# Kernel tuning notes

Hardware: AMD Instinct MI355X
Metric: run time of the kernel (lower is better)

The kernel has to match this reference:

```python
import jax, jax.numpy as jnp
import numpy as np
from jax import lax

EPS = 1e-8  # numerical safety in squash sqrt (torch repo uses plain sqrt)

def squash(s, axis=-1):
    sq = jnp.sum(s * s, axis=axis, keepdims=True)
    return (sq / (1.0 + sq)) * s / jnp.sqrt(sq + EPS)

def conv2d(x, w, b, stride):
    y = lax.conv_general_dilated(x, w, (stride, stride), 'VALID',
                                 dimension_numbers=('NCHW', 'OIHW', 'NCHW'))
    return y + b[None, :, None, None]

def setup_inputs() -> dict:
    key = jax.random.key(0)
    ks = jax.random.split(key, 12)
    B = 256
    x = jax.random.normal(ks[0], (B, 1, 28, 28), dtype=jnp.float32)
    conv_w = jax.random.normal(ks[1], (256, 1, 9, 9), dtype=jnp.float32) * 0.05
    conv_b = jnp.zeros((256,), dtype=jnp.float32)
    caps1_w = jax.random.normal(ks[2], (32, 8, 256, 9, 9), dtype=jnp.float32) * 0.01
    caps1_b = jnp.zeros((32, 8), dtype=jnp.float32)
    caps2_w = jax.random.normal(ks[3], (10, 1152, 8, 16), dtype=jnp.float32)  # torch.randn
    dec_w1 = jax.random.normal(ks[4], (160, 512), dtype=jnp.float32) * 0.05
    dec_b1 = jnp.zeros((512,), dtype=jnp.float32)
    dec_w2 = jax.random.normal(ks[5], (512, 1024), dtype=jnp.float32) * 0.04
    dec_b2 = jnp.zeros((1024,), dtype=jnp.float32)
    dec_w3 = jax.random.normal(ks[6], (1024, 784), dtype=jnp.float32) * 0.03
    dec_b3 = jnp.zeros((784,), dtype=jnp.float32)
    return {"x": x, "conv_w": conv_w, "conv_b": conv_b, "caps1_w": caps1_w,
            "caps1_b": caps1_b, "caps2_w": caps2_w, "dec_w1": dec_w1,
            "dec_b1": dec_b1, "dec_w2": dec_w2, "dec_b2": dec_b2,
            "dec_w3": dec_w3, "dec_b3": dec_b3}

def reference(x, conv_w, conv_b, caps1_w, caps1_b, caps2_w,
              dec_w1, dec_b1, dec_w2, dec_b2, dec_w3, dec_b3):
    B = x.shape[0]
    # conv + relu -> [B,256,20,20]
    h = jax.nn.relu(conv2d(x, conv_w, conv_b, 1))
    # CapsLayerOne: 32 parallel convs folded into one grouped-out conv -> [B,256,6,6]
    u = conv2d(h, caps1_w.reshape(32 * 8, 256, 9, 9), caps1_b.reshape(-1), 2)
    u = u.reshape(B, 32, 8, 6, 6)                    # [B,caps,ch,h,w]
    # replicate torch cat(dim=-1).view(B,8,-1): flatten order (h, caps, w) per channel
    u = u.transpose(0, 2, 3, 1, 4).reshape(B, 8, 1152)  # [B,8,N]
    u = squash(u.transpose(0, 2, 1))                 # [B,N,8], N=1152
    # CapsLayerTwo dynamic routing
    x_hat = jnp.einsum('bni,cnio->cbno', u, caps2_w)[:, :, :, None, :]  # [10,B,N,1,16]
    b = jnp.zeros_like(x_hat)
    v = None
    for i in range(3):
        c = jax.nn.softmax(b, axis=2)
        s = jnp.sum(x_hat * c, axis=2, keepdims=True)  # [10,B,1,1,16]
        v = squash(s)
        if i != 2:
            b = b + jnp.sum(x_hat * v, axis=-1, keepdims=True)
    v = v[:, :, 0, 0, :].transpose(1, 0, 2)            # [B,10,16]
    class_scores = jnp.sqrt(jnp.sum(v * v, axis=-1) + EPS)  # [B,10]
    class_probabilities = jax.nn.softmax(class_scores, axis=-1)
    labels = jnp.argmax(class_probabilities, axis=1)
    y = jax.nn.one_hot(labels, 10, dtype=v.dtype)
    masked = (v * y[:, :, None]).reshape(B, 160)
    d = jax.nn.relu(masked @ dec_w1 + dec_b1)
    d = jax.nn.relu(d @ dec_w2 + dec_b2)
    reconstructions = jax.nn.sigmoid(d @ dec_w3 + dec_b3)  # [B,784]
    return (class_probabilities, reconstructions)
```

## Files before the change

### kernel.cpp

```cpp
#include <hip/hip_runtime.h>
#include <cstdint>
#include <cstddef>

#define EPSF 1e-8f

typedef __attribute__((ext_vector_type(8))) short bf16x8;
typedef __attribute__((ext_vector_type(4))) float f32x4;
typedef unsigned short ushort_t;

static __device__ __forceinline__ ushort_t f2bf(float f) {
  unsigned u = __builtin_bit_cast(unsigned, f);
  unsigned r = (u + 0x7FFFu + ((u >> 16) & 1u)) >> 16;
  return (ushort_t)r;
}
static __device__ __forceinline__ float bf2f(ushort_t h) {
  return __builtin_bit_cast(float, (unsigned)h << 16);
}

__global__ __launch_bounds__(256) void conv1_kernel(
    const float* __restrict__ x, const float* __restrict__ cw,
    const float* __restrict__ cb, ushort_t* __restrict__ h2hi, ushort_t* __restrict__ h2lo)
{
  int oy = blockIdx.x, b = blockIdx.y, ci = threadIdx.x;
  float w[81];
#pragma unroll
  for (int i = 0; i < 81; ++i) w[i] = cw[ci * 81 + i];
  float bias = cb[ci];
  float acc[20];
#pragma unroll
  for (int ox = 0; ox < 20; ++ox) acc[ox] = bias;
  const float* xb = x + (size_t)b * 784;
  for (int ky = 0; ky < 9; ++ky) {
    const float* row = xb + (oy + ky) * 28;
    float rv[28];
#pragma unroll
    for (int c = 0; c < 28; ++c) rv[c] = row[c];
#pragma unroll
    for (int kx = 0; kx < 9; ++kx) {
      float wv = w[ky * 9 + kx];
#pragma unroll
      for (int ox = 0; ox < 20; ++ox)
        acc[ox] = fmaf(rv[ox + kx], wv, acc[ox]);
    }
  }
#pragma unroll
  for (int ox = 0; ox < 20; ++ox) {
    float a = fmaxf(acc[ox], 0.f);
    ushort_t hi = f2bf(a);
    ushort_t lo = f2bf(a - bf2f(hi));
    size_t o = ((size_t)(b * 400 + oy * 20 + ox)) * 256 + ci;
    h2hi[o] = hi; h2lo[o] = lo;
  }
}

__global__ __launch_bounds__(256) void w2k_prep_kernel(
    const float* __restrict__ c1w, ushort_t* __restrict__ w2khi, ushort_t* __restrict__ w2klo)
{
  int co = blockIdx.x, ci = threadIdx.x;
  const float* src = c1w + ((size_t)co * 256 + ci) * 81;
  size_t dst = (size_t)co * 20736 + ci;
  for (int tap = 0; tap < 81; ++tap) {
    float v = src[tap];
    ushort_t hi = f2bf(v);
    w2khi[dst + (size_t)tap * 256] = hi;
    w2klo[dst + (size_t)tap * 256] = f2bf(v - bf2f(hi));
  }
}

__global__ __launch_bounds__(256, 1) void caps1_mfma_kernel(
    const ushort_t* __restrict__ h2hi, const ushort_t* __restrict__ h2lo,
    const ushort_t* __restrict__ w2khi, const ushort_t* __restrict__ w2klo,
    float* __restrict__ partial)
{
  int bid = blockIdx.x;
  int ks8  = bid & 7;
  int ks   = ks8 >> 1;
  int ktap = ks8 & 1;
  int rest = bid >> 3;
  int mt = rest & 1;
  int nt = (rest >> 1) & 1;
  int pos = rest >> 2;
  int ys = pos / 6, xs = pos % 6;
  int t = threadIdx.x;
  int wid = t >> 6, lane = t & 63;
  int wr = wid >> 1, wc = wid & 1;
  int lrow = lane & 15, g = lane >> 4;

  int b0 = mt * 128, n0 = nt * 128, cib = ks * 64;
  int tb    = ktap ? 41 : 0;
  int ntaps = ktap ? 40 : 41;

  __shared__ ushort_t lds[2][4][128 * 64];

  f32x4 acc[4][4];
#pragma unroll
  for (int i = 0; i < 4; ++i)
#pragma unroll
    for (int j = 0; j < 4; ++j) acc[i][j] = (f32x4){0.f, 0.f, 0.f, 0.f};

  int c_ = (t & 7) ^ ((t >> 3) & 7);
  size_t aRow400[4], bRowC[4];
  int ldsBase[4];
#pragma unroll
  for (int i = 0; i < 4; ++i) {
    int row = i * 32 + (t >> 3);
    aRow400[i] = (size_t)(b0 + row) * 400;
    bRowC[i]   = (size_t)(n0 + row) * 20736 + cib + c_ * 8;
    ldsBase[i] = (i * 32 + wid * 8) * 64;
  }

  auto stage = [&](int tap, int bufi) {
    int ky = tap / 9, kx = tap - ky * 9;
    int pix = (2 * ys + ky) * 20 + 2 * xs + kx;
#pragma unroll
    for (int i = 0; i < 4; ++i) {
      size_t ao = (aRow400[i] + pix) * 256 + cib + c_ * 8;
      size_t bo = bRowC[i] + (size_t)tap * 256;
      __builtin_amdgcn_global_load_lds(h2hi + ao, &lds[bufi][0][ldsBase[i]], 16, 0, 0);
      __builtin_amdgcn_global_load_lds(h2lo + ao, &lds[bufi][1][ldsBase[i]], 16, 0, 0);
      __builtin_amdgcn_global_load_lds(w2khi + bo, &lds[bufi][2][ldsBase[i]], 16, 0, 0);
      __builtin_amdgcn_global_load_lds(w2klo + bo, &lds[bufi][3][ldsBase[i]], 16, 0, 0);
    }
  };

  bf16x8 a_h[2][4], a_l[2][4], b_h[2][4], b_l[2][4];

  auto read_frags_k = [&](int kseg, int bufi) {
    const ushort_t* L0 = &lds[bufi][0][0];
    const ushort_t* L1 = &lds[bufi][1][0];
    const ushort_t* L2 = &lds[bufi][2][0];
    const ushort_t* L3 = &lds[bufi][3][0];
#pragma unroll
    for (int f = 0; f < 4; ++f) {
      int ra = wr * 64 + f * 16 + lrow;
      int oa = ra * 64 + ((kseg * 4 + g) ^ (ra & 7)) * 8;
      a_h[kseg][f] = *(const bf16x8*)(L0 + oa);
      a_l[kseg][f] = *(const bf16x8*)(L1 + oa);
      int rb = wc * 64 + f * 16 + lrow;
      int ob = rb * 64 + ((kseg * 4 + g) ^ (rb & 7)) * 8;
      b_h[kseg][f] = *(const bf16x8*)(L2 + ob);
      b_l[kseg][f] = *(const bf16x8*)(L3 + ob);
    }
  };

  auto mfma_kseg = [&](int kseg) {
    __builtin_amdgcn_s_setprio(1);
#pragma unroll
    for (int mf = 0; mf < 4; ++mf)
#pragma unroll
      for (int nf = 0; nf < 4; ++nf) {
        acc[mf][nf] = __builtin_amdgcn_mfma_f32_16x16x32_bf16(a_h[kseg][mf], b_h[kseg][nf], acc[mf][nf], 0, 0, 0);
        acc[mf][nf] = __builtin_amdgcn_mfma_f32_16x16x32_bf16(a_h[kseg][mf], b_l[kseg][nf], acc[mf][nf], 0, 0, 0);
        acc[mf][nf] = __builtin_amdgcn_mfma_f32_16x16x32_bf16(a_l[kseg][mf], b_h[kseg][nf], acc[mf][nf], 0, 0, 0);
      }
    __builtin_amdgcn_s_setprio(0);
  };

  stage(tb + 0, 0);
  stage(tb + 1, 1);
  asm volatile("s_waitcnt vmcnt(16)" ::: "memory");
  __builtin_amdgcn_s_barrier();
  asm volatile("" ::: "memory");
  read_frags_k(0, 0);
  read_frags_k(1, 0);
  asm volatile("s_waitcnt lgkmcnt(0)" ::: "memory");
  __builtin_amdgcn_sched_barrier(0);
  __builtin_amdgcn_s_barrier();
  asm volatile("" ::: "memory");

  for (int j = 0; j < ntaps; ++j) {
    int cur = j & 1;
    if (j + 2 < ntaps) stage(tb + j + 2, cur);
    mfma_kseg(0);
    if (j + 1 < ntaps) {
      if (j + 2 < ntaps) { asm volatile("s_waitcnt vmcnt(16)" ::: "memory"); }
      else               { asm volatile("s_waitcnt vmcnt(0)" ::: "memory"); }
      __builtin_amdgcn_s_barrier();
      asm volatile("" ::: "memory");
      read_frags_k(0, cur ^ 1);
    }
    mfma_kseg(1);
    if (j + 1 < ntaps) read_frags_k(1, cur ^ 1);
    asm volatile("s_waitcnt lgkmcnt(0)" ::: "memory");
    __builtin_amdgcn_sched_barrier(0);
    __builtin_amdgcn_s_barrier();
    asm volatile("" ::: "memory");
  }

  float* pp = partial + (size_t)ks8 * 2359296;
#pragma unroll
  for (int mf = 0; mf < 4; ++mf) {
    int m = b0 + wr * 64 + mf * 16 + g * 4;
#pragma unroll
    for (int nf = 0; nf < 4; ++nf) {
      int n = n0 + wc * 64 + nf * 16 + lrow;
#pragma unroll
      for (int r = 0; r < 4; ++r)
        pp[((size_t)(pos * 256 + m + r)) * 256 + n] = acc[mf][nf][r];
    }
  }
}

__global__ __launch_bounds__(256) void combine_kernel(
    const float* __restrict__ partial, const float* __restrict__ c1b, float* __restrict__ u)
{
  int gidx = blockIdx.x * 256 + threadIdx.x;
  int caps = gidx & 31;
  int b = (gidx >> 5) & 255;
  int pos = gidx >> 13;
  int ys = pos / 6, xs = pos % 6;
  size_t base = ((size_t)pos * 256 + b) * 256 + caps * 8;
  f32x4 s0 = {0.f, 0.f, 0.f, 0.f}, s1 = {0.f, 0.f, 0.f, 0.f};
#pragma unroll
  for (int ksp = 0; ksp < 8; ++ksp) {
    const float* pp = partial + (size_t)ksp * 2359296 + base;
    s0 += *(const f32x4*)pp;
    s1 += *(const f32x4*)(pp + 4);
  }
  const float* bp = c1b + caps * 8;
#pragma unroll
  for (int i = 0; i < 4; ++i) { s0[i] += bp[i]; s1[i] += bp[4 + i]; }
  float sq = s0[0]*s0[0] + s0[1]*s0[1] + s0[2]*s0[2] + s0[3]*s0[3]
           + s1[0]*s1[0] + s1[1]*s1[1] + s1[2]*s1[2] + s1[3]*s1[3];
  float scale = sq / ((1.f + sq) * sqrtf(sq + EPSF));
  int nvec = ys * 192 + caps * 6 + xs;
  float* up = u + ((size_t)b * 1152 + nvec) * 8;
  f32x4 o0, o1;
#pragma unroll
  for (int i = 0; i < 4; ++i) { o0[i] = s0[i] * scale; o1[i] = s1[i] * scale; }
  *(f32x4*)up = o0;
  *(f32x4*)(up + 4) = o1;
}

__global__ __launch_bounds__(320) void xhat_kernel(
    const float* __restrict__ u, const float* __restrict__ W2, float* __restrict__ xh)
{
  int np = blockIdx.x;
  int t = threadIdx.x;
  int nh = t / 160;
  int r  = t % 160;
  int c = r >> 4, o = r & 15;
  int n = np * 2 + nh;
  __shared__ float us[2][256][8];
  for (int e = t; e < 4096; e += 320) {
    int b = e >> 4;
    int nn = (e >> 3) & 1, i = e & 7;
    us[nn][b][i] = u[((size_t)b * 1152 + np * 2 + nn) * 8 + i];
  }
  __syncthreads();
  float wcol[8];
  const float* wp = W2 + (((size_t)c * 1152 + n) * 8) * 16 + o;
#pragma unroll
  for (int i = 0; i < 8; ++i) wcol[i] = wp[i * 16];
  float* xp = xh + ((size_t)(c * 256) * 1152 + n) * 16 + o;
  for (int b = 0; b < 256; ++b) {
    float s = 0.f;
#pragma unroll
    for (int i = 0; i < 8; ++i) s = fmaf(us[nh][b][i], wcol[i], s);
    xp[(size_t)b * 1152 * 16] = s;
  }
}

__global__ __launch_bounds__(256) void routing_kernel(
    const float* __restrict__ xhat, float* __restrict__ vout)
{
  int b = blockIdx.x, c = blockIdx.y, t = threadIdx.x;
  int wid = t >> 6, lane = t & 63;
  float xh[5][16];
  float bn[5] = {0, 0, 0, 0, 0};
  bool valid[5];
  const float* xp = xhat + ((size_t)(c * 256 + b)) * 1152 * 16;
#pragma unroll
  for (int j = 0; j < 5; ++j) {
    int n = t + 256 * j;
    valid[j] = (n < 1152);
    if (valid[j]) {
      const f32x4* q = (const f32x4*)(xp + (size_t)n * 16);
#pragma unroll
      for (int v4 = 0; v4 < 4; ++v4) {
        f32x4 val = q[v4];
#pragma unroll
        for (int k = 0; k < 4; ++k) xh[j][v4 * 4 + k] = val[k];
      }
    } else {
#pragma unroll
      for (int o = 0; o < 16; ++o) xh[j][o] = 0.f;
    }
  }
  __shared__ float redm[4], redz[4], reds[64], sv[16];
  float scale = 0.f;
  for (int it = 0; it < 3; ++it) {
    float m = -1e30f;
#pragma unroll
    for (int j = 0; j < 5; ++j) if (valid[j]) m = fmaxf(m, bn[j]);
    for (int d = 1; d < 64; d <<= 1) m = fmaxf(m, __shfl_xor(m, d));
    if (lane == 0) redm[wid] = m;
    __syncthreads();
    m = fmaxf(fmaxf(redm[0], redm[1]), fmaxf(redm[2], redm[3]));
    float e[5]; float z = 0.f;
#pragma unroll
    for (int j = 0; j < 5; ++j) { e[j] = valid[j] ? expf(bn[j] - m) : 0.f; z += e[j]; }
    for (int d = 1; d < 64; d <<= 1) z += __shfl_xor(z, d);
    if (lane == 0) redz[wid] = z;
    __syncthreads();
    z = redz[0] + redz[1] + redz[2] + redz[3];
    float ps[16];
#pragma unroll
    for (int o = 0; o < 16; ++o) ps[o] = 0.f;
#pragma unroll
    for (int j = 0; j < 5; ++j)
#pragma unroll
      for (int o = 0; o < 16; ++o) ps[o] = fmaf(e[j], xh[j][o], ps[o]);
#pragma unroll
    for (int o = 0; o < 16; ++o) {
      float vv = ps[o];
      for (int d = 1; d < 64; d <<= 1) vv += __shfl_xor(vv, d);
      if (lane == 0) reds[wid * 16 + o] = vv;
    }
    __syncthreads();
    if (t < 16) sv[t] = (reds[t] + reds[16 + t] + reds[32 + t] + reds[48 + t]) / z;
    __syncthreads();
    float vsc[16]; float sq = 0.f;
#pragma unroll
    for (int o = 0; o < 16; ++o) { vsc[o] = sv[o]; sq += sv[o] * sv[o]; }
    scale = sq / ((1.f + sq) * sqrtf(sq + EPSF));
    if (it < 2) {
#pragma unroll
      for (int j = 0; j < 5; ++j) if (valid[j]) {
        float dot = 0.f;
#pragma unroll
        for (int o = 0; o < 16; ++o) dot = fmaf(xh[j][o], vsc[o] * scale, dot);
        bn[j] += dot;
      }
    }
    __syncthreads();
  }
  if (t < 16) vout[((size_t)c * 256 + b) * 16 + t] = sv[t] * scale;
}

__global__ __launch_bounds__(256) void classify_kernel(
    const float* __restrict__ v, float* __restrict__ probs, float* __restrict__ masked)
{
  int b = blockIdx.x, t = threadIdx.x;
  __shared__ float sc[10], vv[160];
  int c = t >> 4, o = t & 15;
  float val = 0.f;
  if (t < 160) { val = v[((size_t)c * 256 + b) * 16 + o]; vv[t] = val; }
  float sq = val * val;
  sq += __shfl_xor(sq, 1); sq += __shfl_xor(sq, 2);
  sq += __shfl_xor(sq, 4); sq += __shfl_xor(sq, 8);
  if (t < 160 && o == 0) sc[c] = sqrtf(sq + EPSF);
  __syncthreads();
  float m = sc[0];
#pragma unroll
  for (int i = 1; i < 10; ++i) m = fmaxf(m, sc[i]);
  float ee[10]; float Z = 0.f;
#pragma unroll
  for (int i = 0; i < 10; ++i) { ee[i] = expf(sc[i] - m); Z += ee[i]; }
  float p[10];
#pragma unroll
  for (int i = 0; i < 10; ++i) p[i] = ee[i] / Z;
  int label = 0; float best = p[0];
#pragma unroll
  for (int i = 1; i < 10; ++i) if (p[i] > best) { best = p[i]; label = i; }
  if (t < 10) probs[(size_t)b * 10 + t] = p[t];
  if (t < 160) masked[(size_t)b * 160 + t] = (c == label) ? vv[t] : 0.f;
}

template <int ACT>
__global__ __launch_bounds__(256) void mlp_kernel(
    const float* __restrict__ A, const float* __restrict__ W,
    const float* __restrict__ bias, float* __restrict__ C, int N, int K)
{
  int j = blockIdx.x * 64 + (threadIdx.x & 63);
  int ty = threadIdx.x >> 6;
  int m0 = blockIdx.y * 16;
  __shared__ float As[16][33];
  float acc[4] = {0.f, 0.f, 0.f, 0.f};
  for (int k0 = 0; k0 < K; k0 += 32) {
    for (int e = threadIdx.x; e < 512; e += 256) {
      int r = e >> 5, kk = e & 31;
      As[r][kk] = A[(size_t)(m0 + r) * K + k0 + kk];
    }
    __syncthreads();
    if (j < N) {
      for (int kk = 0; kk < 32; ++kk) {
        float wv = W[(size_t)(k0 + kk) * N + j];
#pragma unroll
        for (int r = 0; r < 4; ++r) acc[r] = fmaf(As[ty + 4 * r][kk], wv, acc[r]);
      }
    }
    __syncthreads();
  }
  if (j < N) {
    float bv = bias[j];
#pragma unroll
    for (int r = 0; r < 4; ++r) {
      float xx = acc[r] + bv;
      if (ACT == 0) xx = fmaxf(xx, 0.f);
      else xx = 1.f / (1.f + expf(-xx));
      C[(size_t)(m0 + ty + 4 * r) * N + j] = xx;
    }
  }
}

extern "C" void kernel_launch(void* const* d_in, const int* in_sizes, int n_in,
                              void* d_out, int out_size, void* d_ws, size_t ws_size,
                              hipStream_t stream)
{
  const float* x   = (const float*)d_in[0];
  const float* cw  = (const float*)d_in[1];
  const float* cb  = (const float*)d_in[2];
  const float* c1w = (const float*)d_in[3];
  const float* c1b = (const float*)d_in[4];
  const float* c2w = (const float*)d_in[5];
  const float* w1  = (const float*)d_in[6];
  const float* b1  = (const float*)d_in[7];
  const float* w2  = (const float*)d_in[8];
  const float* b2  = (const float*)d_in[9];
  const float* w3  = (const float*)d_in[10];
  const float* b3  = (const float*)d_in[11];
  float* out = (float*)d_out;

  char* p = (char*)d_ws;
  float* xh = (float*)p;
  ushort_t* h2hi  = (ushort_t*)p; p += (size_t)26214400 * 2;
  ushort_t* h2lo  = (ushort_t*)p; p += (size_t)26214400 * 2;
  ushort_t* w2khi = (ushort_t*)p; p += (size_t)5308416 * 2;
  ushort_t* w2klo = (ushort_t*)p; p += (size_t)5308416 * 2;
  float* partial  = (float*)p;    p += (size_t)8 * 2359296 * 4;
  float* u        = (float*)p;    p += (size_t)2359296 * 4;
  float* v        = (float*)p;    p += (size_t)40960 * 4;
  float* masked   = (float*)p;    p += (size_t)40960 * 4;
  float* a1       = (float*)p;    p += (size_t)131072 * 4;
  float* a2       = (float*)p;    p += (size_t)262144 * 4;

  hipLaunchKernelGGL(w2k_prep_kernel, dim3(256), dim3(256), 0, stream, c1w, w2khi, w2klo);
  hipLaunchKernelGGL(conv1_kernel, dim3(20, 256), dim3(256), 0, stream, x, cw, cb, h2hi, h2lo);
  hipLaunchKernelGGL(caps1_mfma_kernel, dim3(1152), dim3(256), 0, stream, h2hi, h2lo, w2khi, w2klo, partial);
  hipLaunchKernelGGL(combine_kernel, dim3(1152), dim3(256), 0, stream, partial, c1b, u);
  hipLaunchKernelGGL(xhat_kernel, dim3(576), dim3(320), 0, stream, u, c2w, xh);
  hipLaunchKernelGGL(routing_kernel, dim3(256, 10), dim3(256), 0, stream, xh, v);
  hipLaunchKernelGGL(classify_kernel, dim3(256), dim3(256), 0, stream, v, out, masked);
  hipLaunchKernelGGL(mlp_kernel<0>, dim3(8, 16), dim3(256), 0, stream, masked, w1, b1, a1, 512, 160);
  hipLaunchKernelGGL(mlp_kernel<0>, dim3(16, 16), dim3(256), 0, stream, a1, w2, b2, a2, 1024, 512);
  hipLaunchKernelGGL(mlp_kernel<1>, dim3(13, 16), dim3(256), 0, stream, a2, w3, b3, out + 2560, 784, 1024);
}
```

Baseline: 664.4 us.

## Interleave hi/lo bf16 planes and halve caps1 LDS for two blocks per CU

The conv1 output and the caps1 weights now store their bf16 hi and lo parts in one buffer, interleaved in 32-channel blocks, so each staged 64-element row holds both hi and lo. This halves the caps1 MFMA kernel's LDS footprint, allowing launch_bounds(256,2) and two resident blocks per CU. The K loop now steps over half-taps with a single fragment set, and the block index order is rearranged. The xhat kernel's thread-to-(c,n,o) mapping also changes so each group of 32 threads writes contiguous output. The finer pipeline adds a barrier per half-tap and keeps fewer loads in flight per block.

```diff
diff --git a/kernel.cpp b/kernel.cpp
--- a/kernel.cpp
+++ b/kernel.cpp
@@ -19,7 +19,7 @@
 
 __global__ __launch_bounds__(256) void conv1_kernel(
     const float* __restrict__ x, const float* __restrict__ cw,
-    const float* __restrict__ cb, ushort_t* __restrict__ h2hi, ushort_t* __restrict__ h2lo)
+    const float* __restrict__ cb, ushort_t* __restrict__ h2x)
 {
   int oy = blockIdx.x, b = blockIdx.y, ci = threadIdx.x;
   float w[81];
@@ -43,54 +43,54 @@
         acc[ox] = fmaf(rv[ox + kx], wv, acc[ox]);
     }
   }
+  int cblk = ci >> 5, jj = ci & 31;
 #pragma unroll
   for (int ox = 0; ox < 20; ++ox) {
     float a = fmaxf(acc[ox], 0.f);
     ushort_t hi = f2bf(a);
     ushort_t lo = f2bf(a - bf2f(hi));
-    size_t o = ((size_t)(b * 400 + oy * 20 + ox)) * 256 + ci;
-    h2hi[o] = hi; h2lo[o] = lo;
+    size_t o = ((size_t)(b * 400 + oy * 20 + ox)) * 512 + cblk * 64 + jj;
+    h2x[o] = hi; h2x[o + 32] = lo;
   }
 }
 
 __global__ __launch_bounds__(256) void w2k_prep_kernel(
-    const float* __restrict__ c1w, ushort_t* __restrict__ w2khi, ushort_t* __restrict__ w2klo)
+    const float* __restrict__ c1w, ushort_t* __restrict__ w2k)
 {
   int co = blockIdx.x, ci = threadIdx.x;
   const float* src = c1w + ((size_t)co * 256 + ci) * 81;
-  size_t dst = (size_t)co * 20736 + ci;
+  int cblk = ci >> 5, jj = ci & 31;
   for (int tap = 0; tap < 81; ++tap) {
     float v = src[tap];
     ushort_t hi = f2bf(v);
-    w2khi[dst + (size_t)tap * 256] = hi;
-    w2klo[dst + (size_t)tap * 256] = f2bf(v - bf2f(hi));
-  }
-}
-
-__global__ __launch_bounds__(256, 1) void caps1_mfma_kernel(
-    const ushort_t* __restrict__ h2hi, const ushort_t* __restrict__ h2lo,
-    const ushort_t* __restrict__ w2khi, const ushort_t* __restrict__ w2klo,
+    size_t dst = ((size_t)co * 81 + tap) * 512 + cblk * 64 + jj;
+    w2k[dst] = hi;
+    w2k[dst + 32] = f2bf(v - bf2f(hi));
+  }
+}
+
+__global__ __launch_bounds__(256, 2) void caps1_mfma_kernel(
+    const ushort_t* __restrict__ h2x, const ushort_t* __restrict__ w2k,
     float* __restrict__ partial)
 {
   int bid = blockIdx.x;
-  int ks8  = bid & 7;
-  int ks   = ks8 >> 1;
-  int ktap = ks8 & 1;
-  int rest = bid >> 3;
-  int mt = rest & 1;
-  int nt = (rest >> 1) & 1;
-  int pos = rest >> 2;
+  int ks = bid & 3;
+  int nt = (bid >> 2) & 1;
+  int kt = (bid >> 3) & 1;
+  int mt = (bid >> 4) & 1;
+  int pos = bid >> 5;
   int ys = pos / 6, xs = pos % 6;
   int t = threadIdx.x;
   int wid = t >> 6, lane = t & 63;
   int wr = wid >> 1, wc = wid & 1;
   int lrow = lane & 15, g = lane >> 4;
 
-  int b0 = mt * 128, n0 = nt * 128, cib = ks * 64;
-  int tb    = ktap ? 41 : 0;
-  int ntaps = ktap ? 40 : 41;
-
-  __shared__ ushort_t lds[2][4][128 * 64];
+  int b0 = mt * 128, n0 = nt * 128;
+  int tb    = kt ? 41 : 0;
+  int ntaps = kt ? 40 : 41;
+  int nht   = 2 * ntaps;
+
+  __shared__ ushort_t lds[2][2][128 * 64];
 
   f32x4 acc[4][4];
 #pragma unroll
@@ -99,95 +99,83 @@
     for (int j = 0; j < 4; ++j) acc[i][j] = (f32x4){0.f, 0.f, 0.f, 0.f};
 
   int c_ = (t & 7) ^ ((t >> 3) & 7);
-  size_t aRow400[4], bRowC[4];
+  size_t aRow400[4], bRow81[4];
   int ldsBase[4];
 #pragma unroll
   for (int i = 0; i < 4; ++i) {
     int row = i * 32 + (t >> 3);
     aRow400[i] = (size_t)(b0 + row) * 400;
-    bRowC[i]   = (size_t)(n0 + row) * 20736 + cib + c_ * 8;
+    bRow81[i]  = (size_t)(n0 + row) * 81;
     ldsBase[i] = (i * 32 + wid * 8) * 64;
   }
 
-  auto stage = [&](int tap, int bufi) {
+  auto stage = [&](int j, int bufi) {
+    int tap = tb + (j >> 1);
+    int cbk = ks * 2 + (j & 1);
     int ky = tap / 9, kx = tap - ky * 9;
     int pix = (2 * ys + ky) * 20 + 2 * xs + kx;
+    int sub = cbk * 64 + c_ * 8;
 #pragma unroll
     for (int i = 0; i < 4; ++i) {
-      size_t ao = (aRow400[i] + pix) * 256 + cib + c_ * 8;
-      size_t bo = bRowC[i] + (size_t)tap * 256;
-      __builtin_amdgcn_global_load_lds(h2hi + ao, &lds[bufi][0][ldsBase[i]], 16, 0, 0);
-      __builtin_amdgcn_global_load_lds(h2lo + ao, &lds[bufi][1][ldsBase[i]], 16, 0, 0);
-      __builtin_amdgcn_global_load_lds(w2khi + bo, &lds[bufi][2][ldsBase[i]], 16, 0, 0);
-      __builtin_amdgcn_global_load_lds(w2klo + bo, &lds[bufi][3][ldsBase[i]], 16, 0, 0);
+      const ushort_t* ga = h2x + (aRow400[i] + pix) * 512 + sub;
+      const ushort_t* gb = w2k + (bRow81[i] + tap) * 512 + sub;
+      __builtin_amdgcn_global_load_lds(ga, &lds[bufi][0][ldsBase[i]], 16, 0, 0);
+      __builtin_amdgcn_global_load_lds(gb, &lds[bufi][1][ldsBase[i]], 16, 0, 0);
     }
   };
 
-  bf16x8 a_h[2][4], a_l[2][4], b_h[2][4], b_l[2][4];
-
-  auto read_frags_k = [&](int kseg, int bufi) {
-    const ushort_t* L0 = &lds[bufi][0][0];
-    const ushort_t* L1 = &lds[bufi][1][0];
-    const ushort_t* L2 = &lds[bufi][2][0];
-    const ushort_t* L3 = &lds[bufi][3][0];
+  bf16x8 a_h[4], a_l[4], b_h[4], b_l[4];
+  auto read_frags = [&](int bufi) {
+    const ushort_t* LA = &lds[bufi][0][0];
+    const ushort_t* LB = &lds[bufi][1][0];
 #pragma unroll
     for (int f = 0; f < 4; ++f) {
       int ra = wr * 64 + f * 16 + lrow;
-      int oa = ra * 64 + ((kseg * 4 + g) ^ (ra & 7)) * 8;
-      a_h[kseg][f] = *(const bf16x8*)(L0 + oa);
-      a_l[kseg][f] = *(const bf16x8*)(L1 + oa);
+      int sa = ra * 64;
+      a_h[f] = *(const bf16x8*)(LA + sa + ((g)     ^ (ra & 7)) * 8);
+      a_l[f] = *(const bf16x8*)(LA + sa + ((4 + g) ^ (ra & 7)) * 8);
       int rb = wc * 64 + f * 16 + lrow;
-      int ob = rb * 64 + ((kseg * 4 + g) ^ (rb & 7)) * 8;
-      b_h[kseg][f] = *(const bf16x8*)(L2 + ob);
-      b_l[kseg][f] = *(const bf16x8*)(L3 + ob);
+      int sb = rb * 64;
+      b_h[f] = *(const bf16x8*)(LB + sb + ((g)     ^ (rb & 7)) * 8);
+      b_l[f] = *(const bf16x8*)(LB + sb + ((4 + g) ^ (rb & 7)) * 8);
     }
   };
 
-  auto mfma_kseg = [&](int kseg) {
-    __builtin_amdgcn_s_setprio(1);
-#pragma unroll
-    for (int mf = 0; mf < 4; ++mf)
-#pragma unroll
-      for (int nf = 0; nf < 4; ++nf) {
-        acc[mf][nf] = __builtin_amdgcn_mfma_f32_16x16x32_bf16(a_h[kseg][mf], b_h[kseg][nf], acc[mf][nf], 0, 0, 0);
-        acc[mf][nf] = __builtin_amdgcn_mfma_f32_16x16x32_bf16(a_h[kseg][mf], b_l[kseg][nf], acc[mf][nf], 0, 0, 0);
-        acc[mf][nf] = __builtin_amdgcn_mfma_f32_16x16x32_bf16(a_l[kseg][mf], b_h[kseg][nf], acc[mf][nf], 0, 0, 0);
-      }
-    __builtin_amdgcn_s_setprio(0);
-  };
-
-  stage(tb + 0, 0);
-  stage(tb + 1, 1);
-  asm volatile("s_waitcnt vmcnt(16)" ::: "memory");
-  __builtin_amdgcn_s_barrier();
-  asm volatile("" ::: "memory");
-  read_frags_k(0, 0);
-  read_frags_k(1, 0);
-  asm volatile("s_waitcnt lgkmcnt(0)" ::: "memory");
+  stage(0, 0);
+  stage(1, 1);
+  asm volatile("s_waitcnt vmcnt(8)" ::: "memory");
   __builtin_amdgcn_sched_barrier(0);
   __builtin_amdgcn_s_barrier();
-  asm volatile("" ::: "memory");
-
-  for (int j = 0; j < ntaps; ++j) {
+
+  for (int j = 0; j < nht; ++j) {
     int cur = j & 1;
-    if (j + 2 < ntaps) stage(tb + j + 2, cur);
-    mfma_kseg(0);
-    if (j + 1 < ntaps) {
-      if (j + 2 < ntaps) { asm volatile("s_waitcnt vmcnt(16)" ::: "memory"); }
-      else               { asm volatile("s_waitcnt vmcnt(0)" ::: "memory"); }
-      __builtin_amdgcn_s_barrier();
-      asm volatile("" ::: "memory");
-      read_frags_k(0, cur ^ 1);
-    }
-    mfma_kseg(1);
-    if (j + 1 < ntaps) read_frags_k(1, cur ^ 1);
+    read_frags(cur);
     asm volatile("s_waitcnt lgkmcnt(0)" ::: "memory");
     __builtin_amdgcn_sched_barrier(0);
     __builtin_amdgcn_s_barrier();
-    asm volatile("" ::: "memory");
-  }
-
-  float* pp = partial + (size_t)ks8 * 2359296;
+
+    if (j + 2 < nht) stage(j + 2, cur);
+    __builtin_amdgcn_sched_barrier(0);
+
+    __builtin_amdgcn_s_setprio(1);
+#pragma unroll
+    for (int mf = 0; mf < 4; ++mf)
+#pragma unroll
+      for (int nf = 0; nf < 4; ++nf) {
+        acc[mf][nf] = __builtin_amdgcn_mfma_f32_16x16x32_bf16(a_h[mf], b_h[nf], acc[mf][nf], 0, 0, 0);
+        acc[mf][nf] = __builtin_amdgcn_mfma_f32_16x16x32_bf16(a_h[mf], b_l[nf], acc[mf][nf], 0, 0, 0);
+        acc[mf][nf] = __builtin_amdgcn_mfma_f32_16x16x32_bf16(a_l[mf], b_h[nf], acc[mf][nf], 0, 0, 0);
+      }
+    __builtin_amdgcn_s_setprio(0);
+    __builtin_amdgcn_sched_barrier(0);
+
+    if (j + 2 < nht) { asm volatile("s_waitcnt vmcnt(8)" ::: "memory"); }
+    else             { asm volatile("s_waitcnt vmcnt(0)" ::: "memory"); }
+    __builtin_amdgcn_sched_barrier(0);
+    __builtin_amdgcn_s_barrier();
+  }
+
+  float* pp = partial + (size_t)(kt * 4 + ks) * 2359296;
 #pragma unroll
   for (int mf = 0; mf < 4; ++mf) {
     int m = b0 + wr * 64 + mf * 16 + g * 4;
@@ -237,9 +225,9 @@
 {
   int np = blockIdx.x;
   int t = threadIdx.x;
-  int nh = t / 160;
-  int r  = t % 160;
-  int c = r >> 4, o = r & 15;
+  int c  = t >> 5;
+  int nh = (t >> 4) & 1;
+  int o  = t & 15;
   int n = np * 2 + nh;
   __shared__ float us[2][256][8];
   for (int e = t; e < 4096; e += 320) {
@@ -424,20 +412,18 @@
 
   char* p = (char*)d_ws;
   float* xh = (float*)p;
-  ushort_t* h2hi  = (ushort_t*)p; p += (size_t)26214400 * 2;
-  ushort_t* h2lo  = (ushort_t*)p; p += (size_t)26214400 * 2;
-  ushort_t* w2khi = (ushort_t*)p; p += (size_t)5308416 * 2;
-  ushort_t* w2klo = (ushort_t*)p; p += (size_t)5308416 * 2;
-  float* partial  = (float*)p;    p += (size_t)8 * 2359296 * 4;
-  float* u        = (float*)p;    p += (size_t)2359296 * 4;
-  float* v        = (float*)p;    p += (size_t)40960 * 4;
-  float* masked   = (float*)p;    p += (size_t)40960 * 4;
-  float* a1       = (float*)p;    p += (size_t)131072 * 4;
-  float* a2       = (float*)p;    p += (size_t)262144 * 4;
-
-  hipLaunchKernelGGL(w2k_prep_kernel, dim3(256), dim3(256), 0, stream, c1w, w2khi, w2klo);
-  hipLaunchKernelGGL(conv1_kernel, dim3(20, 256), dim3(256), 0, stream, x, cw, cb, h2hi, h2lo);
-  hipLaunchKernelGGL(caps1_mfma_kernel, dim3(1152), dim3(256), 0, stream, h2hi, h2lo, w2khi, w2klo, partial);
+  ushort_t* h2x = (ushort_t*)p; p += (size_t)52428800 * 2;
+  ushort_t* w2k = (ushort_t*)p; p += (size_t)10616832 * 2;
+  float* partial = (float*)p;   p += (size_t)8 * 2359296 * 4;
+  float* u       = (float*)p;   p += (size_t)2359296 * 4;
+  float* v       = (float*)p;   p += (size_t)40960 * 4;
+  float* masked  = (float*)p;   p += (size_t)40960 * 4;
+  float* a1      = (float*)p;   p += (size_t)131072 * 4;
+  float* a2      = (float*)p;   p += (size_t)262144 * 4;
+
+  hipLaunchKernelGGL(w2k_prep_kernel, dim3(256), dim3(256), 0, stream, c1w, w2k);
+  hipLaunchKernelGGL(conv1_kernel, dim3(20, 256), dim3(256), 0, stream, x, cw, cb, h2x);
+  hipLaunchKernelGGL(caps1_mfma_kernel, dim3(1152), dim3(256), 0, stream, h2x, w2k, partial);
   hipLaunchKernelGGL(combine_kernel, dim3(1152), dim3(256), 0, stream, partial, c1b, u);
   hipLaunchKernelGGL(xhat_kernel, dim3(576), dim3(320), 0, stream, u, c2w, xh);
   hipLaunchKernelGGL(routing_kernel, dim3(256, 10), dim3(256), 0, stream, xh, v);
```

New measurement: 609.9 us. -8.2%, faster.
